# Kernel optimization log

Measured on AMD Instinct MI355X. Metric: run time of the kernel, lower is better.

The kernel has to match this reference:

```python
import jax, jax.numpy as jnp
import numpy as np

K = 3      # kernel_size
PAD = 1    # padding


def setup_inputs() -> dict:
    key = jax.random.key(0)
    ks = jax.random.split(key, 5)
    B, Cin, Cout, H, W = 8, 64, 64, 128, 128
    x = jax.random.normal(ks[0], (B, Cin, H, W), jnp.float32)
    # offset conv params (zero-init in the module; use small random values so the
    # deformable gather path is actually exercised)
    offset_w = jax.random.normal(ks[1], (2 * K, Cin, K, K), jnp.float32) * 0.01
    offset_b = jax.random.normal(ks[2], (2 * K,), jnp.float32) * 0.01
    # kaiming-normal strip weights
    std = float(np.sqrt(2.0 / (Cin * K)))
    w_h = jax.random.normal(ks[3], (Cout, Cin, 1, K), jnp.float32) * std
    w_v = jax.random.normal(ks[4], (Cout, Cin, K, 1), jnp.float32) * std
    return {"x": x, "offset_w": offset_w, "offset_b": offset_b, "w_h": w_h, "w_v": w_v}


def _bilinear_gather(x, py, px):
    # x: [B,C,H,W]; py, px: [B,K,H,W] float sampling coordinates.
    # Returns bilinearly sampled values [B,C,K,H,W] with zero padding outside.
    B, C, H, W = x.shape
    y0 = jnp.floor(py)
    x0 = jnp.floor(px)
    wy1 = py - y0
    wx1 = px - x0

    def corner(yf, xf, w):
        valid = ((yf >= 0) & (yf <= H - 1) & (xf >= 0) & (xf <= W - 1)).astype(x.dtype)
        yi = jnp.clip(yf, 0, H - 1).astype(jnp.int32)
        xi = jnp.clip(xf, 0, W - 1).astype(jnp.int32)
        v = jax.vmap(lambda im, yy, xx: im[:, yy, xx])(x, yi, xi)  # [B,C,K,H,W]
        return v * (w * valid)[:, None]

    return (corner(y0, x0, (1 - wy1) * (1 - wx1))
            + corner(y0, x0 + 1, (1 - wy1) * wx1)
            + corner(y0 + 1, x0, wy1 * (1 - wx1))
            + corner(y0 + 1, x0 + 1, wy1 * wx1))


def reference(x, offset_w, offset_b, w_h, w_v):
    B, C, H, W = x.shape
    # offset conv (standard 3x3, stride 1, pad 1) -> [B, 2K, H, W]
    off = jax.lax.conv_general_dilated(
        x, offset_w, window_strides=(1, 1), padding=((PAD, PAD), (PAD, PAD)),
        dimension_numbers=("NCHW", "OIHW", "NCHW")) + offset_b[None, :, None, None]
    h_off = off[:, :K]   # per-tap vertical (y) offsets for the horizontal strip
    v_off = off[:, K:]   # per-tap horizontal (x) offsets for the vertical strip

    ygrid = jnp.arange(H, dtype=x.dtype)
    xgrid = jnp.arange(W, dtype=x.dtype)
    taps = jnp.arange(K, dtype=x.dtype) - PAD  # tap displacements along the strip

    # horizontal strip: taps move along x, deform offsets bend the strip in y
    py_h = ygrid[None, None, :, None] + h_off                              # [B,K,H,W]
    px_h = jnp.broadcast_to(xgrid[None, None, None, :] + taps[None, :, None, None],
                            (B, K, H, W))
    val_h = _bilinear_gather(x, py_h, px_h)                                # [B,C,K,H,W]
    out_h = jnp.einsum("bckhw,ock->bohw", val_h, w_h[:, :, 0, :])

    # vertical strip: taps move along y, deform offsets bend the strip in x
    py_v = jnp.broadcast_to(ygrid[None, None, :, None] + taps[None, :, None, None],
                            (B, K, H, W))
    px_v = xgrid[None, None, None, :] + v_off
    val_v = _bilinear_gather(x, py_v, px_v)
    out_v = jnp.einsum("bckhw,ock->bohw", val_v, w_v[:, :, :, 0])

    return out_h + out_v
```

## Files before the change

### kernel.cpp

```cpp
#include <hip/hip_runtime.h>

#define HH 128
#define WW 128
#define HW (HH * WW)
#define CIN 64
#define COUT 64

#define XT_OFF  0
#define BF_OFF  16777216
#define OBF_OFF (BF_OFF + 49152)

typedef short bf16x8 __attribute__((ext_vector_type(8)));
typedef float f32x4 __attribute__((ext_vector_type(4)));

__device__ __forceinline__ unsigned short f2bf(float f) {
    union { float f; unsigned int u; } v; v.f = f;
    unsigned int r = v.u + 0x7FFFu + ((v.u >> 16) & 1u);
    return (unsigned short)(r >> 16);
}
__device__ __forceinline__ float bf2f(unsigned short u) {
    union { unsigned int u; float f; } v; v.u = ((unsigned int)u) << 16;
    return v.f;
}

__global__ __launch_bounds__(256) void prep_kernel(const float* __restrict__ ow,
                                                   const float* __restrict__ wh,
                                                   const float* __restrict__ wv,
                                                   unsigned short* __restrict__ Bf,
                                                   unsigned short* __restrict__ OBf) {
    int i = blockIdx.x * 256 + threadIdx.x;
    if (i < 24576) {
        int j    = i & 7;
        int lane = (i >> 3) & 63;
        int nt   = (i >> 9) & 3;
        int kc   = (i >> 11) & 1;
        int pk   = i >> 12;
        int o = nt * 16 + (lane & 15);
        int c = kc * 32 + (lane >> 4) * 8 + j;
        int k = pk % 3;
        const float* src = (pk < 3) ? wh : wv;
        Bf[i] = f2bf(src[(o * CIN + c) * 3 + k]);
    } else if (i < 24576 + 9216) {
        int mI   = i - 24576;
        int j    = mI & 7;
        int lane = (mI >> 3) & 63;
        int s    = mI >> 9;
        int n    = lane & 15;
        int q    = lane >> 4;
        int c    = (s & 1) * 32 + q * 8 + j;
        int tap  = s >> 1;
        int dy   = tap / 3, dx = tap % 3;
        OBf[mI] = (n < 6) ? f2bf(ow[((n * CIN + c) * 3 + dy) * 3 + dx])
                          : (unsigned short)0;
    }
}

__global__ __launch_bounds__(256) void repack_kernel(const float* __restrict__ x,
                                                     unsigned short* __restrict__ xT) {
    __shared__ float tile[64 * 129];
    const int tid = threadIdx.x;
    const int blk = blockIdx.x;
    const int b   = blk & 7;
    const int y   = blk >> 3;

    const float* xb = x + (size_t)b * CIN * HW + y * WW;
    const int tx = tid & 127;
    const int th = tid >> 7;
    for (int c0 = 0; c0 < 64; c0 += 2) {
        int c = c0 + th;
        tile[c * 129 + tx] = xb[(size_t)c * HW + tx];
    }
    __syncthreads();

    unsigned short* ob = xT + ((size_t)b * HW + y * WW) * 64;
#pragma unroll
    for (int it = 0; it < 4; ++it) {
        int e  = it * 256 + tid;
        int h  = e & 7;
        int px = e >> 3;
        union { unsigned short us[8]; uint4 u4; } pkd;
#pragma unroll
        for (int j = 0; j < 8; ++j)
            pkd.us[j] = f2bf(tile[(h * 8 + j) * 129 + px]);
        *(uint4*)&ob[px * 64 + h * 8] = pkd.u4;
    }
}

__global__ __launch_bounds__(256) void fused_kernel(const unsigned short* __restrict__ xT,
                                                    const float* __restrict__ obias,
                                                    const unsigned short* __restrict__ Bf,
                                                    const unsigned short* __restrict__ OBf,
                                                    float* __restrict__ out) {
    __shared__ float offT[4 * 32 * 9];

    const int tid  = threadIdx.x;
    const int w    = tid >> 6;
    const int lane = tid & 63;
    const int q    = lane >> 4;
    const int m    = lane & 15;

    const int blk = blockIdx.x;
    const int b   = blk & 7;
    const int y   = blk >> 3;
    const int x0w = w << 5;

    const unsigned short* xtb = xT + (size_t)b * HW * 64;

    f32x4 acc6[2] = {{0.f, 0.f, 0.f, 0.f}, {0.f, 0.f, 0.f, 0.f}};
#pragma unroll
    for (int s = 0; s < 18; ++s) {
        const int tap  = s >> 1;
        const int dy   = tap / 3 - 1;
        const int dx   = tap % 3 - 1;
        const int coff = (s & 1) * 32 + q * 8;
        bf16x8 bfr = *(const bf16x8*)&OBf[(s * 64 + lane) * 8];
#pragma unroll
        for (int mt = 0; mt < 2; ++mt) {
            int yy = y + dy;
            int xx = x0w + mt * 16 + m + dx;
            bool ok = (yy >= 0) && (yy < HH) && (xx >= 0) && (xx < WW);
            int yc = min(max(yy, 0), HH - 1);
            int xc = min(max(xx, 0), WW - 1);
            uint4 raw = *(const uint4*)&xtb[(size_t)(yc * WW + xc) * 64 + coff];
            if (!ok) raw = make_uint4(0, 0, 0, 0);
            union { uint4 u4; bf16x8 v; } af; af.u4 = raw;
            acc6[mt] = __builtin_amdgcn_mfma_f32_16x16x32_bf16(af.v, bfr, acc6[mt], 0, 0, 0);
        }
    }
    float bias = (m < 6) ? obias[m] : 0.f;
#pragma unroll
    for (int mt = 0; mt < 2; ++mt)
#pragma unroll
        for (int reg = 0; reg < 4; ++reg)
            if (m < 6) offT[(w * 32 + mt * 16 + q * 4 + reg) * 9 + m] = acc6[mt][reg] + bias;
    __syncthreads();

    f32x4 acc[2][4];
#pragma unroll
    for (int mt = 0; mt < 2; ++mt)
#pragma unroll
        for (int nt = 0; nt < 4; ++nt) acc[mt][nt] = (f32x4){0.f, 0.f, 0.f, 0.f};

#pragma unroll
    for (int pk = 0; pk < 6; ++pk) {
        const int ph = pk / 3;
        const int k  = pk % 3;

        float wA[2], wB[2];
        const unsigned short *pA[2], *pB[2];
#pragma unroll
        for (int mt = 0; mt < 2; ++mt) {
            const int xs = x0w + mt * 16 + m;
            float o1 = offT[(w * 32 + mt * 16 + m) * 9 + pk];
            int idxA, idxB;
            if (ph == 0) {
                float py  = (float)y + o1;
                float y0f = floorf(py);
                float wy  = py - y0f;
                int   yi  = (int)y0f;
                bool v0 = (yi >= 0) && (yi <= HH - 1);
                bool v1 = (yi + 1 >= 0) && (yi + 1 <= HH - 1);
                int  pxx = xs + k - 1;
                bool pv  = (pxx >= 0) && (pxx <= WW - 1);
                wA[mt] = (pv && v0) ? (1.f - wy) : 0.f;
                wB[mt] = (pv && v1) ? wy : 0.f;
                int ra = min(max(yi, 0), HH - 1);
                int rb = min(max(yi + 1, 0), HH - 1);
                int ca = min(max(pxx, 0), WW - 1);
                idxA = ra * WW + ca;
                idxB = rb * WW + ca;
            } else {
                float pxf = (float)xs + o1;
                float x0f = floorf(pxf);
                float wx  = pxf - x0f;
                int   xi  = (int)x0f;
                bool v0 = (xi >= 0) && (xi <= WW - 1);
                bool v1 = (xi + 1 >= 0) && (xi + 1 <= WW - 1);
                int  py = y + k - 1;
                bool pv = (py >= 0) && (py <= HH - 1);
                wA[mt] = (pv && v0) ? (1.f - wx) : 0.f;
                wB[mt] = (pv && v1) ? wx : 0.f;
                int ra  = min(max(py, 0), HH - 1);
                int ca  = min(max(xi, 0), WW - 1);
                int cb2 = min(max(xi + 1, 0), WW - 1);
                idxA = ra * WW + ca;
                idxB = ra * WW + cb2;
            }
            pA[mt] = xtb + (size_t)idxA * 64;
            pB[mt] = xtb + (size_t)idxB * 64;
        }

#pragma unroll
        for (int kc = 0; kc < 2; ++kc) {
            const int coff = kc * 32 + q * 8;
            bf16x8 afrag[2];
#pragma unroll
            for (int mt = 0; mt < 2; ++mt) {
                union { uint4 u4; unsigned short us[8]; bf16x8 v; } ua, ub, uf;
                ua.u4 = *(const uint4*)(pA[mt] + coff);
                ub.u4 = *(const uint4*)(pB[mt] + coff);
#pragma unroll
                for (int j = 0; j < 8; ++j) {
                    float v = wA[mt] * bf2f(ua.us[j]) + wB[mt] * bf2f(ub.us[j]);
                    uf.us[j] = f2bf(v);
                }
                afrag[mt] = uf.v;
            }
#pragma unroll
            for (int nt = 0; nt < 4; ++nt) {
                bf16x8 bfr = *(const bf16x8*)&Bf[(((pk * 2 + kc) * 4 + nt) * 64 + lane) * 8];
#pragma unroll
                for (int mt = 0; mt < 2; ++mt)
                    acc[mt][nt] = __builtin_amdgcn_mfma_f32_16x16x32_bf16(
                        afrag[mt], bfr, acc[mt][nt], 0, 0, 0);
            }
        }
    }

#pragma unroll
    for (int mt = 0; mt < 2; ++mt)
#pragma unroll
        for (int nt = 0; nt < 4; ++nt) {
            int o = nt * 16 + m;
            float* op = out + ((size_t)(b * COUT + o) * HH + y) * WW + x0w + mt * 16 + q * 4;
            *(f32x4*)op = acc[mt][nt];
        }
}

extern "C" void kernel_launch(void* const* d_in, const int* in_sizes, int n_in,
                              void* d_out, int out_size, void* d_ws, size_t ws_size,
                              hipStream_t stream) {
    const float* x     = (const float*)d_in[0];
    const float* ow    = (const float*)d_in[1];
    const float* obias = (const float*)d_in[2];
    const float* wh    = (const float*)d_in[3];
    const float* wv    = (const float*)d_in[4];
    float* out = (float*)d_out;

    char* ws = (char*)d_ws;
    unsigned short* xT  = (unsigned short*)(ws + XT_OFF);
    unsigned short* Bf  = (unsigned short*)(ws + BF_OFF);
    unsigned short* OBf = (unsigned short*)(ws + OBF_OFF);

    prep_kernel<<<dim3(132), dim3(256), 0, stream>>>(ow, wh, wv, Bf, OBf);
    repack_kernel<<<dim3(1024), dim3(256), 0, stream>>>(x, xT);
    fused_kernel<<<dim3(1024), dim3(256), 0, stream>>>(xT, obias, Bf, OBf, out);
}
```

Baseline: 138.8 us.

## Merge prep into repack kernel and halve per-block work in fused kernel

Folds the weight-prep kernel into the repack kernel as extra blocks, removing one launch. The fused kernel now handles 16 pixels per wave instead of 32, so each block covers half a row and the grid doubles to 2048 blocks. Launch bounds now request 6 blocks per SM, and all six bilinear index and weight sets are computed before the MFMA loop. The bilinear result is rounded to bf16 with a cheaper round-half-up conversion, which can differ slightly from round-to-nearest-even. The aim is higher occupancy and lower register pressure, at the cost of reloading B fragments per 16-pixel tile.

New measurement: 143.4 us. +3.3%, slower.

```diff
diff --git a/kernel.cpp b/kernel.cpp
--- a/kernel.cpp
+++ b/kernel.cpp
@@ -18,80 +18,84 @@
     unsigned int r = v.u + 0x7FFFu + ((v.u >> 16) & 1u);
     return (unsigned short)(r >> 16);
 }
+__device__ __forceinline__ unsigned short f2bf_up(float f) {
+    union { float f; unsigned int u; } v; v.f = f;
+    return (unsigned short)((v.u + 0x8000u) >> 16);
+}
 __device__ __forceinline__ float bf2f(unsigned short u) {
     union { unsigned int u; float f; } v; v.u = ((unsigned int)u) << 16;
     return v.f;
 }
 
-__global__ __launch_bounds__(256) void prep_kernel(const float* __restrict__ ow,
-                                                   const float* __restrict__ wh,
-                                                   const float* __restrict__ wv,
-                                                   unsigned short* __restrict__ Bf,
-                                                   unsigned short* __restrict__ OBf) {
-    int i = blockIdx.x * 256 + threadIdx.x;
-    if (i < 24576) {
-        int j    = i & 7;
-        int lane = (i >> 3) & 63;
-        int nt   = (i >> 9) & 3;
-        int kc   = (i >> 11) & 1;
-        int pk   = i >> 12;
-        int o = nt * 16 + (lane & 15);
-        int c = kc * 32 + (lane >> 4) * 8 + j;
-        int k = pk % 3;
-        const float* src = (pk < 3) ? wh : wv;
-        Bf[i] = f2bf(src[(o * CIN + c) * 3 + k]);
-    } else if (i < 24576 + 9216) {
-        int mI   = i - 24576;
-        int j    = mI & 7;
-        int lane = (mI >> 3) & 63;
-        int s    = mI >> 9;
-        int n    = lane & 15;
-        int q    = lane >> 4;
-        int c    = (s & 1) * 32 + q * 8 + j;
-        int tap  = s >> 1;
-        int dy   = tap / 3, dx = tap % 3;
-        OBf[mI] = (n < 6) ? f2bf(ow[((n * CIN + c) * 3 + dy) * 3 + dx])
-                          : (unsigned short)0;
-    }
-}
-
-__global__ __launch_bounds__(256) void repack_kernel(const float* __restrict__ x,
-                                                     unsigned short* __restrict__ xT) {
+__global__ __launch_bounds__(256) void prep_repack_kernel(const float* __restrict__ x,
+                                                          const float* __restrict__ ow,
+                                                          const float* __restrict__ wh,
+                                                          const float* __restrict__ wv,
+                                                          unsigned short* __restrict__ xT,
+                                                          unsigned short* __restrict__ Bf,
+                                                          unsigned short* __restrict__ OBf) {
     __shared__ float tile[64 * 129];
     const int tid = threadIdx.x;
     const int blk = blockIdx.x;
-    const int b   = blk & 7;
-    const int y   = blk >> 3;
-
-    const float* xb = x + (size_t)b * CIN * HW + y * WW;
-    const int tx = tid & 127;
-    const int th = tid >> 7;
-    for (int c0 = 0; c0 < 64; c0 += 2) {
-        int c = c0 + th;
-        tile[c * 129 + tx] = xb[(size_t)c * HW + tx];
-    }
-    __syncthreads();
-
-    unsigned short* ob = xT + ((size_t)b * HW + y * WW) * 64;
-#pragma unroll
-    for (int it = 0; it < 4; ++it) {
-        int e  = it * 256 + tid;
-        int h  = e & 7;
-        int px = e >> 3;
-        union { unsigned short us[8]; uint4 u4; } pkd;
-#pragma unroll
-        for (int j = 0; j < 8; ++j)
-            pkd.us[j] = f2bf(tile[(h * 8 + j) * 129 + px]);
-        *(uint4*)&ob[px * 64 + h * 8] = pkd.u4;
-    }
-}
-
-__global__ __launch_bounds__(256) void fused_kernel(const unsigned short* __restrict__ xT,
-                                                    const float* __restrict__ obias,
-                                                    const unsigned short* __restrict__ Bf,
-                                                    const unsigned short* __restrict__ OBf,
-                                                    float* __restrict__ out) {
-    __shared__ float offT[4 * 32 * 9];
+
+    if (blk < 1024) {
+        const int b = blk & 7;
+        const int y = blk >> 3;
+        const float* xb = x + (size_t)b * CIN * HW + y * WW;
+        const int tx = tid & 127;
+        const int th = tid >> 7;
+        for (int c0 = 0; c0 < 64; c0 += 2) {
+            int c = c0 + th;
+            tile[c * 129 + tx] = xb[(size_t)c * HW + tx];
+        }
+        __syncthreads();
+        unsigned short* ob = xT + ((size_t)b * HW + y * WW) * 64;
+#pragma unroll
+        for (int it = 0; it < 4; ++it) {
+            int e  = it * 256 + tid;
+            int h  = e & 7;
+            int px = e >> 3;
+            union { unsigned short us[8]; uint4 u4; } pkd;
+#pragma unroll
+            for (int j = 0; j < 8; ++j)
+                pkd.us[j] = f2bf(tile[(h * 8 + j) * 129 + px]);
+            *(uint4*)&ob[px * 64 + h * 8] = pkd.u4;
+        }
+    } else {
+        int i = (blk - 1024) * 256 + tid;
+        if (i < 24576) {
+            int j    = i & 7;
+            int lane = (i >> 3) & 63;
+            int nt   = (i >> 9) & 3;
+            int kc   = (i >> 11) & 1;
+            int pk   = i >> 12;
+            int o = nt * 16 + (lane & 15);
+            int c = kc * 32 + (lane >> 4) * 8 + j;
+            int k = pk % 3;
+            const float* src = (pk < 3) ? wh : wv;
+            Bf[i] = f2bf(src[(o * CIN + c) * 3 + k]);
+        } else if (i < 24576 + 9216) {
+            int mI   = i - 24576;
+            int j    = mI & 7;
+            int lane = (mI >> 3) & 63;
+            int s    = mI >> 9;
+            int n    = lane & 15;
+            int q    = lane >> 4;
+            int c    = (s & 1) * 32 + q * 8 + j;
+            int tap  = s >> 1;
+            int dy   = tap / 3, dx = tap % 3;
+            OBf[mI] = (n < 6) ? f2bf(ow[((n * CIN + c) * 3 + dy) * 3 + dx])
+                              : (unsigned short)0;
+        }
+    }
+}
+
+__global__ __launch_bounds__(256, 6) void fused_kernel(const unsigned short* __restrict__ xT,
+                                                       const float* __restrict__ obias,
+                                                       const unsigned short* __restrict__ Bf,
+                                                       const unsigned short* __restrict__ OBf,
+                                                       float* __restrict__ out) {
+    __shared__ float offT[4 * 16 * 8];
 
     const int tid  = threadIdx.x;
     const int w    = tid >> 6;
@@ -101,130 +105,116 @@
 
     const int blk = blockIdx.x;
     const int b   = blk & 7;
-    const int y   = blk >> 3;
-    const int x0w = w << 5;
+    const int y   = (blk >> 3) & 127;
+    const int xh  = blk >> 10;
+    const int x0w = (xh << 6) + (w << 4);
 
     const unsigned short* xtb = xT + (size_t)b * HW * 64;
 
-    f32x4 acc6[2] = {{0.f, 0.f, 0.f, 0.f}, {0.f, 0.f, 0.f, 0.f}};
+    f32x4 acc6 = {0.f, 0.f, 0.f, 0.f};
 #pragma unroll
     for (int s = 0; s < 18; ++s) {
         const int tap  = s >> 1;
         const int dy   = tap / 3 - 1;
         const int dx   = tap % 3 - 1;
         const int coff = (s & 1) * 32 + q * 8;
+        int yy = y + dy;
+        int xx = x0w + m + dx;
+        bool ok = (yy >= 0) && (yy < HH) && (xx >= 0) && (xx < WW);
+        int yc = min(max(yy, 0), HH - 1);
+        int xc = min(max(xx, 0), WW - 1);
+        uint4 raw = *(const uint4*)&xtb[(size_t)(yc * WW + xc) * 64 + coff];
+        if (!ok) raw = make_uint4(0, 0, 0, 0);
+        union { uint4 u4; bf16x8 v; } af; af.u4 = raw;
         bf16x8 bfr = *(const bf16x8*)&OBf[(s * 64 + lane) * 8];
-#pragma unroll
-        for (int mt = 0; mt < 2; ++mt) {
-            int yy = y + dy;
-            int xx = x0w + mt * 16 + m + dx;
-            bool ok = (yy >= 0) && (yy < HH) && (xx >= 0) && (xx < WW);
-            int yc = min(max(yy, 0), HH - 1);
-            int xc = min(max(xx, 0), WW - 1);
-            uint4 raw = *(const uint4*)&xtb[(size_t)(yc * WW + xc) * 64 + coff];
-            if (!ok) raw = make_uint4(0, 0, 0, 0);
-            union { uint4 u4; bf16x8 v; } af; af.u4 = raw;
-            acc6[mt] = __builtin_amdgcn_mfma_f32_16x16x32_bf16(af.v, bfr, acc6[mt], 0, 0, 0);
-        }
-    }
-    float bias = (m < 6) ? obias[m] : 0.f;
-#pragma unroll
-    for (int mt = 0; mt < 2; ++mt)
+        acc6 = __builtin_amdgcn_mfma_f32_16x16x32_bf16(af.v, bfr, acc6, 0, 0, 0);
+    }
+    if (m < 6) {
+        float bias = obias[m];
 #pragma unroll
         for (int reg = 0; reg < 4; ++reg)
-            if (m < 6) offT[(w * 32 + mt * 16 + q * 4 + reg) * 9 + m] = acc6[mt][reg] + bias;
+            offT[(w * 16 + q * 4 + reg) * 8 + m] = acc6[reg] + bias;
+    }
     __syncthreads();
-
-    f32x4 acc[2][4];
-#pragma unroll
-    for (int mt = 0; mt < 2; ++mt)
-#pragma unroll
-        for (int nt = 0; nt < 4; ++nt) acc[mt][nt] = (f32x4){0.f, 0.f, 0.f, 0.f};
-
+    f32x4  o03 = *(const f32x4*)&offT[(w * 16 + m) * 8];
+    float2 o45 = *(const float2*)&offT[(w * 16 + m) * 8 + 4];
+    float offs[6] = {o03[0], o03[1], o03[2], o03[3], o45.x, o45.y};
+
+    const int xs = x0w + m;
+    float wA[6], wB[6];
+    int   iA[6], iB[6];
 #pragma unroll
     for (int pk = 0; pk < 6; ++pk) {
         const int ph = pk / 3;
         const int k  = pk % 3;
-
-        float wA[2], wB[2];
-        const unsigned short *pA[2], *pB[2];
-#pragma unroll
-        for (int mt = 0; mt < 2; ++mt) {
-            const int xs = x0w + mt * 16 + m;
-            float o1 = offT[(w * 32 + mt * 16 + m) * 9 + pk];
-            int idxA, idxB;
-            if (ph == 0) {
-                float py  = (float)y + o1;
-                float y0f = floorf(py);
-                float wy  = py - y0f;
-                int   yi  = (int)y0f;
-                bool v0 = (yi >= 0) && (yi <= HH - 1);
-                bool v1 = (yi + 1 >= 0) && (yi + 1 <= HH - 1);
-                int  pxx = xs + k - 1;
-                bool pv  = (pxx >= 0) && (pxx <= WW - 1);
-                wA[mt] = (pv && v0) ? (1.f - wy) : 0.f;
-                wB[mt] = (pv && v1) ? wy : 0.f;
-                int ra = min(max(yi, 0), HH - 1);
-                int rb = min(max(yi + 1, 0), HH - 1);
-                int ca = min(max(pxx, 0), WW - 1);
-                idxA = ra * WW + ca;
-                idxB = rb * WW + ca;
-            } else {
-                float pxf = (float)xs + o1;
-                float x0f = floorf(pxf);
-                float wx  = pxf - x0f;
-                int   xi  = (int)x0f;
-                bool v0 = (xi >= 0) && (xi <= WW - 1);
-                bool v1 = (xi + 1 >= 0) && (xi + 1 <= WW - 1);
-                int  py = y + k - 1;
-                bool pv = (py >= 0) && (py <= HH - 1);
-                wA[mt] = (pv && v0) ? (1.f - wx) : 0.f;
-                wB[mt] = (pv && v1) ? wx : 0.f;
-                int ra  = min(max(py, 0), HH - 1);
-                int ca  = min(max(xi, 0), WW - 1);
-                int cb2 = min(max(xi + 1, 0), WW - 1);
-                idxA = ra * WW + ca;
-                idxB = ra * WW + cb2;
-            }
-            pA[mt] = xtb + (size_t)idxA * 64;
-            pB[mt] = xtb + (size_t)idxB * 64;
-        }
-
+        float o1 = offs[pk];
+        if (ph == 0) {
+            float py  = (float)y + o1;
+            float y0f = floorf(py);
+            float wy  = py - y0f;
+            int   yi  = (int)y0f;
+            bool v0 = (yi >= 0) && (yi <= HH - 1);
+            bool v1 = (yi + 1 >= 0) && (yi + 1 <= HH - 1);
+            int  pxx = xs + k - 1;
+            bool pv  = (pxx >= 0) && (pxx <= WW - 1);
+            wA[pk] = (pv && v0) ? (1.f - wy) : 0.f;
+            wB[pk] = (pv && v1) ? wy : 0.f;
+            int ra = min(max(yi, 0), HH - 1);
+            int rb = min(max(yi + 1, 0), HH - 1);
+            int ca = min(max(pxx, 0), WW - 1);
+            iA[pk] = ra * WW + ca;
+            iB[pk] = rb * WW + ca;
+        } else {
+            float pxf = (float)xs + o1;
+            float x0f = floorf(pxf);
+            float wx  = pxf - x0f;
+            int   xi  = (int)x0f;
+            bool v0 = (xi >= 0) && (xi <= WW - 1);
+            bool v1 = (xi + 1 >= 0) && (xi + 1 <= WW - 1);
+            int  py = y + k - 1;
+            bool pv = (py >= 0) && (py <= HH - 1);
+            wA[pk] = (pv && v0) ? (1.f - wx) : 0.f;
+            wB[pk] = (pv && v1) ? wx : 0.f;
+            int ra  = min(max(py, 0), HH - 1);
+            int ca  = min(max(xi, 0), WW - 1);
+            int cb2 = min(max(xi + 1, 0), WW - 1);
+            iA[pk] = ra * WW + ca;
+            iB[pk] = ra * WW + cb2;
+        }
+    }
+
+    f32x4 acc[4];
+#pragma unroll
+    for (int nt = 0; nt < 4; ++nt) acc[nt] = (f32x4){0.f, 0.f, 0.f, 0.f};
+
+#pragma unroll
+    for (int pk = 0; pk < 6; ++pk) {
 #pragma unroll
         for (int kc = 0; kc < 2; ++kc) {
             const int coff = kc * 32 + q * 8;
-            bf16x8 afrag[2];
-#pragma unroll
-            for (int mt = 0; mt < 2; ++mt) {
-                union { uint4 u4; unsigned short us[8]; bf16x8 v; } ua, ub, uf;
-                ua.u4 = *(const uint4*)(pA[mt] + coff);
-                ub.u4 = *(const uint4*)(pB[mt] + coff);
-#pragma unroll
-                for (int j = 0; j < 8; ++j) {
-                    float v = wA[mt] * bf2f(ua.us[j]) + wB[mt] * bf2f(ub.us[j]);
-                    uf.us[j] = f2bf(v);
-                }
-                afrag[mt] = uf.v;
+            union { uint4 u4; unsigned short us[8]; } ua, ub;
+            ua.u4 = *(const uint4*)&xtb[(size_t)iA[pk] * 64 + coff];
+            ub.u4 = *(const uint4*)&xtb[(size_t)iB[pk] * 64 + coff];
+            union { unsigned short us[8]; bf16x8 v; } uf;
+#pragma unroll
+            for (int j = 0; j < 8; ++j) {
+                float v = wA[pk] * bf2f(ua.us[j]) + wB[pk] * bf2f(ub.us[j]);
+                uf.us[j] = f2bf_up(v);
             }
 #pragma unroll
             for (int nt = 0; nt < 4; ++nt) {
                 bf16x8 bfr = *(const bf16x8*)&Bf[(((pk * 2 + kc) * 4 + nt) * 64 + lane) * 8];
-#pragma unroll
-                for (int mt = 0; mt < 2; ++mt)
-                    acc[mt][nt] = __builtin_amdgcn_mfma_f32_16x16x32_bf16(
-                        afrag[mt], bfr, acc[mt][nt], 0, 0, 0);
+                acc[nt] = __builtin_amdgcn_mfma_f32_16x16x32_bf16(uf.v, bfr, acc[nt], 0, 0, 0);
             }
         }
     }
 
 #pragma unroll
-    for (int mt = 0; mt < 2; ++mt)
-#pragma unroll
-        for (int nt = 0; nt < 4; ++nt) {
-            int o = nt * 16 + m;
-            float* op = out + ((size_t)(b * COUT + o) * HH + y) * WW + x0w + mt * 16 + q * 4;
-            *(f32x4*)op = acc[mt][nt];
-        }
+    for (int nt = 0; nt < 4; ++nt) {
+        int o = nt * 16 + m;
+        float* op = out + ((size_t)(b * COUT + o) * HH + y) * WW + x0w + q * 4;
+        *(f32x4*)op = acc[nt];
+    }
 }
 
 extern "C" void kernel_launch(void* const* d_in, const int* in_sizes, int n_in,
@@ -242,7 +232,6 @@
     unsigned short* Bf  = (unsigned short*)(ws + BF_OFF);
     unsigned short* OBf = (unsigned short*)(ws + OBF_OFF);
 
-    prep_kernel<<<dim3(132), dim3(256), 0, stream>>>(ow, wh, wv, Bf, OBf);
-    repack_kernel<<<dim3(1024), dim3(256), 0, stream>>>(x, xT);
-    fused_kernel<<<dim3(1024), dim3(256), 0, stream>>>(xT, obias, Bf, OBf, out);
-}
+    prep_repack_kernel<<<dim3(1156), dim3(256), 0, stream>>>(x, ow, wh, wv, xT, Bf, OBf);
+    fused_kernel<<<dim3(2048), dim3(256), 0, stream>>>(xT, obias, Bf, OBf, out);
+}
```
